# Kernel optimization log

Measured on AMD Instinct MI355X. Metric: run time of the kernel, lower is better.

## Reference

```python
import jax, jax.numpy as jnp
import numpy as np

BLOCK_LEN = 64

def setup_inputs() -> dict:
    key = jax.random.key(0)
    k1, k2, k3, k4 = jax.random.split(key, 4)
    b, s, h, p, n = 2, 4096, 16, 64, 128
    X = jax.random.normal(k1, (b, s, h, p), dtype=jnp.float32)
    # A scaled down so exp(cumsum) of the per-chunk decays stays finite in fp32
    A = jax.random.normal(k2, (b, s, h), dtype=jnp.float32) * 0.02
    B = jax.random.normal(k3, (b, s, h, n), dtype=jnp.float32)
    C = jax.random.normal(k4, (b, s, h, n), dtype=jnp.float32)
    return {"X": X, "A": A, "B": B, "C": C}

def reference(X, A, B, C):
    b, s, h, p = X.shape
    n = B.shape[-1]
    c = s // BLOCK_LEN
    # chunk the sequence: b (c l) ... -> b c l ...
    Xb = X.reshape(b, c, BLOCK_LEN, h, p)
    Bb = B.reshape(b, c, BLOCK_LEN, h, n)
    Ab = A.reshape(b, c, BLOCK_LEN, h).transpose(0, 3, 1, 2)  # b h c l
    A_cumsum = jnp.cumsum(Ab, axis=-1)                         # b h c l
    # decay from each position to the end of its chunk
    decay_states = jnp.exp(A_cumsum[..., -1:] - A_cumsum)      # b h c l
    # per-chunk states (end-of-chunk SSM state contribution)
    states = jnp.einsum('bclhn,bhcl,bclhp->bchpn', Bb, decay_states, Xb)
    init = jnp.zeros_like(states[:, :1])
    states = jnp.concatenate([init, states], axis=1)           # b (c+1) h p n
    # inter-chunk recurrence: only the LAST row of segsum_exp(pad(last_acum))
    # is consumed by new_states[:, -1]; row z=C equals exp(total - cumsum).
    last_acum = A_cumsum[..., -1]                              # b h c
    pad = jnp.pad(last_acum, ((0, 0), (0, 0), (1, 0)))         # b h (c+1)
    cp = jnp.cumsum(pad, axis=-1)
    decay_last = jnp.exp(cp[..., -1:] - cp)                    # b h (c+1)
    # final state after the whole sequence
    return jnp.einsum('bhc,bchpn->bhpn', decay_last, states)
```

## Files before the change

### kernel.cpp

```cpp
#include <hip/hip_runtime.h>
#include <hip/hip_bf16.h>

#define SLEN 4096
#define NH 16
#define PDIM 64
#define NDIM 128
#define NBH 32
#define KSPLIT 16
#define TT 64

typedef __attribute__((ext_vector_type(8))) short short8;
typedef __attribute__((ext_vector_type(4))) float f32x4;

__device__ __forceinline__ int swz(int r) { return ((r & 7) ^ ((r >> 2) & 7)) << 4; }

__device__ __forceinline__ unsigned short f2bfu(float x) {
    __hip_bfloat16 h = __float2bfloat16(x);
    return *reinterpret_cast<unsigned short*>(&h);
}
__device__ __forceinline__ unsigned pack2(float lo, float hi) {
    return (unsigned)f2bfu(lo) | ((unsigned)f2bfu(hi) << 16);
}

template <int KB, int NT>
__global__ __launch_bounds__(512) void state_gemm_kernel(
    const float* __restrict__ X, const float* __restrict__ Bm,
    const float* __restrict__ A, float* __restrict__ partial) {
    int ks = blockIdx.x;
    int bh = blockIdx.y;
    int b = bh >> 4, h = bh & 15;
    int tid = threadIdx.x;
    int lane = tid & 63, wid = tid >> 6;
    int wp = wid & 1, wn = wid >> 1;
    int p0 = wp * 32, n0 = wn * 32;
    int m = lane & 15, kg = lane >> 4;

    __shared__ __align__(16) char lds[2][24576];
    __shared__ float scratch[512];
    __shared__ float wlds[KB];

    int cx = tid & 15, tpx = tid >> 4;
    int cb = tid & 31, tpb = tid >> 5;

    const float* Xb = X + (size_t)b * SLEN * NH * PDIM + (size_t)h * PDIM;
    const float* Bb = Bm + (size_t)b * SLEN * NH * NDIM + (size_t)h * NDIM;
    const float* Ab = A + (size_t)b * SLEN * NH + h;
    int t0 = ks * KB;

    const float* xsrc = Xb + (size_t)(t0 + 2 * tpx) * (NH * PDIM) + 4 * cx;
    const float* bsrc = Bb + (size_t)(t0 + 2 * tpb) * (NH * NDIM) + 4 * cb;

    int wX[4], wB0[4], wB1[4];
#pragma unroll
    for (int i = 0; i < 4; ++i) {
        int rx = 4 * cx + i;
        wX[i] = (rx * 128 + 4 * tpx) ^ swz(rx);
        int rb = 4 * cb + i;
        wB0[i] = 8192 + ((rb * 128 + 4 * tpb) ^ swz(rb));
        wB1[i] = 8192 + ((rb * 128 + 4 * (tpb + 16)) ^ swz(rb));
    }
    int rA[2][2], rB[2][2];
#pragma unroll
    for (int pi = 0; pi < 2; ++pi)
#pragma unroll
        for (int kk = 0; kk < 2; ++kk) {
            int r = p0 + pi * 16 + m;
            rA[pi][kk] = (r * 128 + kk * 64 + kg * 16) ^ swz(r);
        }
#pragma unroll
    for (int ni = 0; ni < 2; ++ni)
#pragma unroll
        for (int kk = 0; kk < 2; ++kk) {
            int rn = n0 + ni * 16 + m;
            rB[ni][kk] = 8192 + ((rn * 128 + kk * 64 + kg * 16) ^ swz(rn));
        }

    f32x4 acc[2][2];
#pragma unroll
    for (int i = 0; i < 2; ++i)
#pragma unroll
        for (int j = 0; j < 2; ++j) acc[i][j] = (f32x4){0.f, 0.f, 0.f, 0.f};

    f32x4 xr0, xr1, br[2][2];
    float wv0, wv1;

#define LOADR(it)                                                              \
    {                                                                          \
        size_t ax = (size_t)(it) * (TT * NH * PDIM);                           \
        size_t ab = (size_t)(it) * (TT * NH * NDIM);                           \
        xr0 = *(const f32x4*)(xsrc + ax);                                      \
        xr1 = *(const f32x4*)(xsrc + ax + NH * PDIM);                          \
        br[0][0] = *(const f32x4*)(bsrc + ab);                                 \
        br[0][1] = *(const f32x4*)(bsrc + ab + NH * NDIM);                     \
        br[1][0] = *(const f32x4*)(bsrc + ab + 32 * NH * NDIM);                \
        br[1][1] = *(const f32x4*)(bsrc + ab + 33 * NH * NDIM);                \
    }

#define LOADW(it)                                                              \
    {                                                                          \
        wv0 = wlds[(it) * TT + 2 * tpx];                                       \
        wv1 = wlds[(it) * TT + 2 * tpx + 1];                                   \
    }

#define CVTW(buf)                                                              \
    {                                                                          \
        char* dst = lds[buf];                                                  \
        _Pragma("unroll") for (int i = 0; i < 4; ++i) {                        \
            *(unsigned*)(dst + wX[i]) = pack2(xr0[i] * wv0, xr1[i] * wv1);     \
            *(unsigned*)(dst + wB0[i]) = pack2(br[0][0][i], br[0][1][i]);      \
            *(unsigned*)(dst + wB1[i]) = pack2(br[1][0][i], br[1][1][i]);      \
        }                                                                      \
    }

#define COMPUTE(buf)                                                           \
    {                                                                          \
        const char* src = lds[buf];                                            \
        short8 af[2][2], bf[2][2];                                             \
        _Pragma("unroll") for (int pi = 0; pi < 2; ++pi)                       \
            _Pragma("unroll") for (int kk = 0; kk < 2; ++kk)                   \
                af[pi][kk] = *(const short8*)(src + rA[pi][kk]);               \
        _Pragma("unroll") for (int ni = 0; ni < 2; ++ni)                       \
            _Pragma("unroll") for (int kk = 0; kk < 2; ++kk)                   \
                bf[ni][kk] = *(const short8*)(src + rB[ni][kk]);               \
        _Pragma("unroll") for (int kk = 0; kk < 2; ++kk)                       \
            _Pragma("unroll") for (int pi = 0; pi < 2; ++pi)                   \
                _Pragma("unroll") for (int ni = 0; ni < 2; ++ni)               \
                    acc[pi][ni] = __builtin_amdgcn_mfma_f32_16x16x32_bf16(     \
                        af[pi][kk], bf[ni][kk], acc[pi][ni], 0, 0, 0);         \
    }

    LOADR(0);

    {
        float s = 0.f;
        for (int t = t0 + KB + tid; t < SLEN; t += 512) s += Ab[(size_t)t * NH];
        scratch[tid] = s;
        __syncthreads();
        for (int off = 256; off > 0; off >>= 1) {
            if (tid < off) scratch[tid] += scratch[tid + off];
            __syncthreads();
        }
        float Stail = scratch[0];
        __syncthreads();

        constexpr int E = (KB + 511) / 512;
        float loc[E > 0 ? E : 1];
        float run = 0.f;
        int base = tid * E;
#pragma unroll
        for (int e = 0; e < E; ++e) {
            int idx = base + e;
            if (idx < KB) { run += Ab[(size_t)(t0 + idx) * NH]; loc[e] = run; }
        }
        scratch[tid] = run;
        __syncthreads();
        for (int off = 1; off < 512; off <<= 1) {
            float v = (tid >= off) ? scratch[tid - off] : 0.f;
            __syncthreads();
            scratch[tid] += v;
            __syncthreads();
        }
        float incl = scratch[tid];
        float tot = scratch[511];
        float excl = incl - run;
        float basew = Stail + tot;
#pragma unroll
        for (int e = 0; e < E; ++e) {
            int idx = base + e;
            if (idx < KB) wlds[idx] = expf(basew - (excl + loc[e]));
        }
        __syncthreads();
    }

    LOADW(0);
    CVTW(0);
    __syncthreads();
    int cur = 0;
    for (int it = 0; it < NT; ++it) {
        if (it + 1 < NT) LOADR(it + 1);
        COMPUTE(cur);
        __syncthreads();
        if (it + 1 < NT) {
            LOADW(it + 1);
            CVTW(cur ^ 1);
        }
        __syncthreads();
        cur ^= 1;
    }
#undef LOADR
#undef LOADW
#undef CVTW
#undef COMPUTE

    float* outp = partial + ((size_t)ks * NBH + bh) * (PDIM * NDIM);
#pragma unroll
    for (int pi = 0; pi < 2; ++pi)
#pragma unroll
        for (int ni = 0; ni < 2; ++ni)
#pragma unroll
            for (int r = 0; r < 4; ++r) {
                int p = p0 + pi * 16 + kg * 4 + r;
                int n = n0 + ni * 16 + m;
                outp[p * NDIM + n] = acc[pi][ni][r];
            }
}

__global__ void reduce_kernel(const float* __restrict__ partial, float* __restrict__ out,
                              int ksplit) {
    int i = blockIdx.x * 256 + threadIdx.x;
    const f32x4* pp = (const f32x4*)partial;
    f32x4 s = (f32x4){0.f, 0.f, 0.f, 0.f};
    for (int ks = 0; ks < ksplit; ++ks) {
        f32x4 v = pp[(size_t)ks * (NBH * PDIM * NDIM / 4) + i];
        s.x += v.x; s.y += v.y; s.z += v.z; s.w += v.w;
    }
    ((f32x4*)out)[i] = s;
}

extern "C" void kernel_launch(void* const* d_in, const int* in_sizes, int n_in,
                              void* d_out, int out_size, void* d_ws, size_t ws_size,
                              hipStream_t stream) {
    const float* X = (const float*)d_in[0];
    const float* A = (const float*)d_in[1];
    const float* Bm = (const float*)d_in[2];
    float* out = (float*)d_out;

    float* partial = (float*)d_ws;
    size_t slice_bytes = (size_t)NBH * PDIM * NDIM * sizeof(float);

    if (ws_size < (size_t)KSPLIT * slice_bytes) {
        state_gemm_kernel<SLEN, SLEN / TT><<<dim3(1, NBH), 512, 0, stream>>>(X, Bm, A, out);
        return;
    }
    state_gemm_kernel<SLEN / KSPLIT, SLEN / KSPLIT / TT>
        <<<dim3(KSPLIT, NBH), 512, 0, stream>>>(X, Bm, A, partial);
    int nout4 = NBH * PDIM * NDIM / 4;
    reduce_kernel<<<nout4 / 256, 256, 0, stream>>>(partial, out, KSPLIT);
}
```

Baseline: 32.02 us.

## Deepen global prefetch to two stages, use warp-shuffle scans, drop one barrier per iteration

```diff
diff --git a/kernel.cpp b/kernel.cpp
--- a/kernel.cpp
+++ b/kernel.cpp
@@ -23,41 +23,35 @@
 }
 
 template <int KB, int NT>
-__global__ __launch_bounds__(512) void state_gemm_kernel(
+__global__ __launch_bounds__(512, 4) void state_gemm_kernel(
     const float* __restrict__ X, const float* __restrict__ Bm,
     const float* __restrict__ A, float* __restrict__ partial) {
     int ks = blockIdx.x;
     int bh = blockIdx.y;
     int b = bh >> 4, h = bh & 15;
     int tid = threadIdx.x;
-    int lane = tid & 63, wid = tid >> 6;
-    int wp = wid & 1, wn = wid >> 1;
+    int lane = tid & 63, wv_ = tid >> 6;
+    int wp = wv_ & 1, wn = wv_ >> 1;
     int p0 = wp * 32, n0 = wn * 32;
     int m = lane & 15, kg = lane >> 4;
+    int c = tid & 15, tp = tid >> 4;
 
     __shared__ __align__(16) char lds[2][24576];
-    __shared__ float scratch[512];
     __shared__ float wlds[KB];
 
-    int cx = tid & 15, tpx = tid >> 4;
-    int cb = tid & 31, tpb = tid >> 5;
-
-    const float* Xb = X + (size_t)b * SLEN * NH * PDIM + (size_t)h * PDIM;
-    const float* Bb = Bm + (size_t)b * SLEN * NH * NDIM + (size_t)h * NDIM;
-    const float* Ab = A + (size_t)b * SLEN * NH + h;
+    const float* Xb = X + (size_t)b * (SLEN * NH * PDIM) + h * PDIM;
+    const float* Bb = Bm + (size_t)b * (SLEN * NH * NDIM) + h * NDIM;
+    const float* Ab = A + (size_t)b * (SLEN * NH) + h;
     int t0 = ks * KB;
 
-    const float* xsrc = Xb + (size_t)(t0 + 2 * tpx) * (NH * PDIM) + 4 * cx;
-    const float* bsrc = Bb + (size_t)(t0 + 2 * tpb) * (NH * NDIM) + 4 * cb;
-
-    int wX[4], wB0[4], wB1[4];
+    const float* xsrc = Xb + (size_t)(t0 + 2 * tp) * (NH * PDIM) + 4 * c;
+    const float* bsrc = Bb + (size_t)(t0 + 2 * tp) * (NH * NDIM) + 4 * c;
+
+    int wX[4];
 #pragma unroll
     for (int i = 0; i < 4; ++i) {
-        int rx = 4 * cx + i;
-        wX[i] = (rx * 128 + 4 * tpx) ^ swz(rx);
-        int rb = 4 * cb + i;
-        wB0[i] = 8192 + ((rb * 128 + 4 * tpb) ^ swz(rb));
-        wB1[i] = 8192 + ((rb * 128 + 4 * (tpb + 16)) ^ swz(rb));
+        int r = 4 * c + i;
+        wX[i] = (r * 128 + 4 * tp) ^ swz(r);
     }
     int rA[2][2], rB[2][2];
 #pragma unroll
@@ -81,34 +75,29 @@
 #pragma unroll
         for (int j = 0; j < 2; ++j) acc[i][j] = (f32x4){0.f, 0.f, 0.f, 0.f};
 
-    f32x4 xr0, xr1, br[2][2];
-    float wv0, wv1;
-
-#define LOADR(it)                                                              \
+    f32x4 rx0[2], rx1[2], rb00[2], rb01[2], rb10[2], rb11[2];
+
+#define LOADR(it, bk)                                                          \
     {                                                                          \
-        size_t ax = (size_t)(it) * (TT * NH * PDIM);                           \
-        size_t ab = (size_t)(it) * (TT * NH * NDIM);                           \
-        xr0 = *(const f32x4*)(xsrc + ax);                                      \
-        xr1 = *(const f32x4*)(xsrc + ax + NH * PDIM);                          \
-        br[0][0] = *(const f32x4*)(bsrc + ab);                                 \
-        br[0][1] = *(const f32x4*)(bsrc + ab + NH * NDIM);                     \
-        br[1][0] = *(const f32x4*)(bsrc + ab + 32 * NH * NDIM);                \
-        br[1][1] = *(const f32x4*)(bsrc + ab + 33 * NH * NDIM);                \
-    }
-
-#define LOADW(it)                                                              \
+        const float* xp = xsrc + (size_t)(it) * (TT * NH * PDIM);              \
+        const float* bp = bsrc + (size_t)(it) * (TT * NH * NDIM);              \
+        rx0[bk] = *(const f32x4*)(xp);                                         \
+        rx1[bk] = *(const f32x4*)(xp + NH * PDIM);                             \
+        rb00[bk] = *(const f32x4*)(bp);                                        \
+        rb01[bk] = *(const f32x4*)(bp + NH * NDIM);                            \
+        rb10[bk] = *(const f32x4*)(bp + 64);                                   \
+        rb11[bk] = *(const f32x4*)(bp + NH * NDIM + 64);                       \
+    }
+
+#define CVTW(buf, bk, it)                                                      \
     {                                                                          \
-        wv0 = wlds[(it) * TT + 2 * tpx];                                       \
-        wv1 = wlds[(it) * TT + 2 * tpx + 1];                                   \
-    }
-
-#define CVTW(buf)                                                              \
-    {                                                                          \
+        float wv0 = wlds[(it) * TT + 2 * tp];                                  \
+        float wv1 = wlds[(it) * TT + 2 * tp + 1];                              \
         char* dst = lds[buf];                                                  \
         _Pragma("unroll") for (int i = 0; i < 4; ++i) {                        \
-            *(unsigned*)(dst + wX[i]) = pack2(xr0[i] * wv0, xr1[i] * wv1);     \
-            *(unsigned*)(dst + wB0[i]) = pack2(br[0][0][i], br[0][1][i]);      \
-            *(unsigned*)(dst + wB1[i]) = pack2(br[1][0][i], br[1][1][i]);      \
+            *(unsigned*)(dst + wX[i]) = pack2(rx0[bk][i] * wv0, rx1[bk][i] * wv1); \
+            *(unsigned*)(dst + wX[i] + 8192) = pack2(rb00[bk][i], rb01[bk][i]);    \
+            *(unsigned*)(dst + wX[i] + 16384) = pack2(rb10[bk][i], rb11[bk][i]);   \
         }                                                                      \
     }
 
@@ -129,22 +118,15 @@
                         af[pi][kk], bf[ni][kk], acc[pi][ni], 0, 0, 0);         \
     }
 
-    LOADR(0);
+    LOADR(0, 0);
+    if (NT > 1) LOADR(1, 1);
 
     {
-        float s = 0.f;
-        for (int t = t0 + KB + tid; t < SLEN; t += 512) s += Ab[(size_t)t * NH];
-        scratch[tid] = s;
-        __syncthreads();
-        for (int off = 256; off > 0; off >>= 1) {
-            if (tid < off) scratch[tid] += scratch[tid + off];
-            __syncthreads();
-        }
-        float Stail = scratch[0];
-        __syncthreads();
-
+        float* sc = (float*)(lds[1]);
+        float ts = 0.f;
+        for (int t = t0 + KB + tid; t < SLEN; t += 512) ts += Ab[(size_t)t * NH];
         constexpr int E = (KB + 511) / 512;
-        float loc[E > 0 ? E : 1];
+        float loc[E];
         float run = 0.f;
         int base = tid * E;
 #pragma unroll
@@ -152,18 +134,27 @@
             int idx = base + e;
             if (idx < KB) { run += Ab[(size_t)(t0 + idx) * NH]; loc[e] = run; }
         }
-        scratch[tid] = run;
+        float v = run;
+#pragma unroll
+        for (int off = 1; off < 64; off <<= 1) {
+            float u = __shfl_up(v, off, 64);
+            if (lane >= off) v += u;
+        }
+#pragma unroll
+        for (int off = 32; off > 0; off >>= 1) ts += __shfl_xor(ts, off, 64);
+        if (lane == 63) sc[wv_] = v;
+        if (lane == 0) sc[8 + wv_] = ts;
         __syncthreads();
-        for (int off = 1; off < 512; off <<= 1) {
-            float v = (tid >= off) ? scratch[tid - off] : 0.f;
-            __syncthreads();
-            scratch[tid] += v;
-            __syncthreads();
-        }
-        float incl = scratch[tid];
-        float tot = scratch[511];
-        float excl = incl - run;
-        float basew = Stail + tot;
+        float woff = 0.f, tot = 0.f, stail = 0.f;
+#pragma unroll
+        for (int q = 0; q < 8; ++q) {
+            float s_ = sc[q];
+            tot += s_;
+            if (q < wv_) woff += s_;
+            stail += sc[8 + q];
+        }
+        float excl = woff + v - run;
+        float basew = stail + tot;
 #pragma unroll
         for (int e = 0; e < E; ++e) {
             int idx = base + e;
@@ -172,23 +163,17 @@
         __syncthreads();
     }
 
-    LOADW(0);
-    CVTW(0);
+    CVTW(0, 0, 0);
     __syncthreads();
-    int cur = 0;
+
+#pragma unroll
     for (int it = 0; it < NT; ++it) {
-        if (it + 1 < NT) LOADR(it + 1);
-        COMPUTE(cur);
+        if (it + 2 < NT) LOADR(it + 2, it & 1);
+        COMPUTE(it & 1);
+        if (it + 1 < NT) CVTW((it + 1) & 1, (it + 1) & 1, it + 1);
         __syncthreads();
-        if (it + 1 < NT) {
-            LOADW(it + 1);
-            CVTW(cur ^ 1);
-        }
-        __syncthreads();
-        cur ^= 1;
     }
 #undef LOADR
-#undef LOADW
 #undef CVTW
 #undef COMPUTE
 
```

After: 29.85 us. -6.8%, faster.
